# Performance work log

Measured on AMD Instinct MI355X. Metric: run time of the kernel, lower is better.

## Reference

```python
import jax, jax.numpy as jnp
import numpy as np

BATCH, INPUTDIM, OUTDIM, GRIDSIZE = 4096, 256, 256, 64


def setup_inputs() -> dict:
    key = jax.random.key(0)
    k1, k2 = jax.random.split(key)
    x = jax.random.normal(k1, (BATCH, INPUTDIM), dtype=jnp.float32)
    # xavier_uniform over (2, outdim, inputdim, gridsize): fan_in = inputdim*gridsize, fan_out = outdim*gridsize
    fan_in = INPUTDIM * GRIDSIZE
    fan_out = OUTDIM * GRIDSIZE
    limit = float(np.sqrt(6.0 / (fan_in + fan_out)))
    fouriercoeffs = jax.random.uniform(
        k2, (2, OUTDIM, INPUTDIM, GRIDSIZE), dtype=jnp.float32,
        minval=-limit, maxval=limit)
    bias = jnp.zeros((1, OUTDIM), dtype=jnp.float32)
    return {"x": x, "fouriercoeffs": fouriercoeffs, "bias": bias}


def reference(x, fouriercoeffs, bias):
    # x: [B, inputdim]; fouriercoeffs: [2, outdim, inputdim, gridsize]; bias: [1, outdim]
    # gridsize_param is clamp/round'ed to an int in torch -> static = initial_gridsize here.
    G = fouriercoeffs.shape[-1]
    k = jnp.arange(1, G + 1, dtype=x.dtype)        # [G] frequencies 1..G
    xk = x[:, :, None] * k                          # [B, inputdim, G]
    c = jnp.cos(xk)                                 # [B, inputdim, G]
    s = jnp.sin(xk)                                 # [B, inputdim, G]
    # Fused contraction over (inputdim, gridsize) -- avoids the naive
    # [B, outdim, inputdim, gridsize] broadcast tensor of the torch code.
    y = (jnp.einsum('big,oig->bo', c, fouriercoeffs[0])
         + jnp.einsum('big,oig->bo', s, fouriercoeffs[1])
         + bias)                                    # [B, outdim]
    return y
```

## Files before the change

kernel.cpp:

```cpp
#include <hip/hip_runtime.h>
#include <hip/hip_bf16.h>


typedef __attribute__((ext_vector_type(8))) short short8;
typedef __attribute__((ext_vector_type(4))) float f32x4;

#define SPLITK 8
#define ICHUNK (256 / SPLITK)

#define INV2PI 0.15915494309189535f

#if __has_builtin(__builtin_amdgcn_cvt_pk_bf16_f32)
typedef __attribute__((ext_vector_type(2))) __bf16 bf16x2_t;
__device__ __forceinline__ unsigned pkbf16(float a, float b) {
    bf16x2_t v = __builtin_amdgcn_cvt_pk_bf16_f32(a, b);
    return __builtin_bit_cast(unsigned, v);
}
#else
__device__ __forceinline__ unsigned pkbf16(float a, float b) {
    unsigned ua = __builtin_bit_cast(unsigned, a) + 0x8000u;
    unsigned ub = __builtin_bit_cast(unsigned, b) + 0x8000u;
    return __builtin_amdgcn_perm(ub, ua, 0x07060302u);
}
#endif

__device__ __forceinline__ void dbl2(float c, float s, float& co, float& so) {
    float t = c + c;
    co = __builtin_fmaf(t, c, -1.f);
    so = t * s;
}
__device__ __forceinline__ void rot2(float c, float s, float cr, float sr,
                                     float& co, float& so) {
    float t = s * sr;
    co = __builtin_fmaf(c, cr, -t);
    float u = s * cr;
    so = __builtin_fmaf(c, sr, u);
}

__device__ __forceinline__ short8 chain8(float m1, float fm1, float f0) {
    unsigned r[4];
    float vp = fm1, v = f0;
    #pragma unroll
    for (int h = 0; h < 4; ++h) {
        float v1 = __builtin_fmaf(m1, v, -vp);
        r[h] = pkbf16(v, v1);
        float v2 = __builtin_fmaf(m1, v1, -v);
        vp = v1; v = v2;
    }
    uint4 u; u.x = r[0]; u.y = r[1]; u.z = r[2]; u.w = r[3];
    return __builtin_bit_cast(short8, u);
}

__device__ __forceinline__ void async_load16(const void* g, void* l) {
    __builtin_amdgcn_global_load_lds(
        (const __attribute__((address_space(1))) unsigned int*)g,
        (__attribute__((address_space(3))) unsigned int*)l,
        16, 0, 0);
}

__global__ void init_out_kernel(float* __restrict__ out, const float* __restrict__ bias) {
    int tid = blockIdx.x * 256 + threadIdx.x;
    float4 b4 = ((const float4*)bias)[tid & 63];
    ((float4*)out)[tid] = b4;
}

__global__ __launch_bounds__(256) void convert_coeffs3(
    const float* __restrict__ fc, unsigned short* __restrict__ ws2)
{
    unsigned flat = blockIdx.x * 256 + threadIdx.x;
    unsigned bx = flat >> 11, gi = flat & 2047;
    unsigned i = bx >> 1, y = bx & 1;
    unsigned sog = gi >> 6, ll = gi & 63;
    unsigned s = sog >> 3, og = sog & 7;
    unsigned op = og * 16 + (ll & 15);
    unsigned k = s * 32 + ((ll >> 4) * 8);
    unsigned tt = k >> 6, g0 = k & 63;
    const float4* src = (const float4*)(fc +
        ((((size_t)tt * 256 + y * 128 + op) * 256 + i) * 64 + g0));
    float4 a = src[0], b = src[1];
    uint4 v;
    v.x = pkbf16(a.x, a.y); v.y = pkbf16(a.z, a.w);
    v.z = pkbf16(b.x, b.y); v.w = pkbf16(b.z, b.w);
    ((uint4*)ws2)[flat] = v;
}

template <bool USE_WS>
__global__ __launch_bounds__(256, 2) void fkan_gemm(
    const float* __restrict__ x, const float* __restrict__ fc,
    const unsigned short* __restrict__ bws, float* __restrict__ out)
{
    __shared__ uint4 Bimg[2][2048];
    __shared__ float xs[ICHUNK][128];

    const int t  = threadIdx.x;
    const int l  = t & 63;
    const int w  = t >> 6;
    const int wr = w >> 1, wc = w & 1;
    const int q  = l >> 4;
    const int m  = l & 15;
    const int rowBase = blockIdx.x * 128;
    const int by      = blockIdx.y;
    const int colBase = by * 128;
    const int iBase   = blockIdx.z * ICHUNK;

    f32x4 acc[4][4];
    #pragma unroll
    for (int a = 0; a < 4; ++a)
        #pragma unroll
        for (int b = 0; b < 4; ++b) acc[a][b] = (f32x4)0.0f;

    auto stageB = [&](int p, int i) {
        if (USE_WS) {
            const unsigned short* base = bws + ((size_t)(i * 2 + by) * 2048) * 8;
            #pragma unroll
            for (int cc = 0; cc < 8; ++cc) {
                int c = cc * 4 + w;
                async_load16(base + (size_t)(c * 64 + l) * 8, (void*)(&Bimg[p][c * 64]));
            }
        } else {
            #pragma unroll
            for (int gg = 0; gg < 8; ++gg) {
                int gi  = gg * 256 + t;
                int sog = gi >> 6, ll = gi & 63;
                int s = sog >> 3, ogb = sog & 7;
                int o = ogb * 16 + (ll & 15);
                int k = s * 32 + (ll >> 4) * 8;
                int tt = k >> 6, g = k & 63;
                const float4* p4 = (const float4*)(fc +
                    ((((size_t)tt * 256 + colBase + o) * 256 + i) * 64 + g));
                float4 a = p4[0], b = p4[1];
                uint4 v;
                v.x = pkbf16(a.x, a.y); v.y = pkbf16(a.z, a.w);
                v.z = pkbf16(b.x, b.y); v.w = pkbf16(b.z, b.w);
                Bimg[p][gi] = v;
            }
        }
    };

    stageB(0, iBase);
    {
        int r = t >> 1, c0 = (t & 1) * 16;
        const float4* px = (const float4*)(x + (size_t)(rowBase + r) * 256 + iBase + c0);
        float4 v0 = px[0], v1 = px[1], v2 = px[2], v3 = px[3];
        float tmp[16] = { v0.x, v0.y, v0.z, v0.w, v1.x, v1.y, v1.z, v1.w,
                          v2.x, v2.y, v2.z, v2.w, v3.x, v3.y, v3.z, v3.w };
        #pragma unroll
        for (int j = 0; j < 16; ++j) xs[c0 + j][r] = tmp[j];
    }
    __syncthreads();

    #pragma unroll 1
    for (int ii = 0; ii < ICHUNK; ++ii) {
        const int p = ii & 1;

        short8 bF[4][4];
        #pragma unroll
        for (int s = 0; s < 4; ++s)
            #pragma unroll
            for (int cf = 0; cf < 4; ++cf)
                bF[s][cf] = __builtin_bit_cast(short8,
                    Bimg[p][(s * 8 + wc * 4 + cf) * 64 + l]);

        if (ii + 1 < ICHUNK) stageB(p ^ 1, iBase + ii + 1);

        short8 aF[4][4];
        #pragma unroll
        for (int rf = 0; rf < 4; ++rf) {
            float xv = xs[ii][wr * 64 + rf * 16 + m];
            float rev = xv * INV2PI;
            float s1 = __builtin_amdgcn_sinf(rev);
            float c1 = __builtin_amdgcn_cosf(rev);
            const float m1 = c1 + c1;
            float c2, s2, c4, s4, c8, s8, c16, s16, c32, s32;
            dbl2(c1, s1, c2, s2);
            dbl2(c2, s2, c4, s4);
            dbl2(c4, s4, c8, s8);
            dbl2(c8, s8, c16, s16);
            dbl2(c16, s16, c32, s32);
            float c24, s24;
            rot2(c16, s16, c8, s8, c24, s24);
            float cq = (q == 0) ? 1.f : (q == 1) ? c8 : (q == 2) ? c16 : c24;
            float sq = (q == 0) ? 0.f : (q == 1) ? s8 : (q == 2) ? s16 : s24;
            float cq1, sq1, cB, sB, cB1, sB1;
            rot2(cq, sq, c1, s1, cq1, sq1);
            rot2(cq, sq, c32, s32, cB, sB);
            rot2(cB, sB, c1, s1, cB1, sB1);
            aF[rf][0] = chain8(m1, cq, cq1);
            aF[rf][1] = chain8(m1, cB, cB1);
            aF[rf][2] = chain8(m1, sq, sq1);
            aF[rf][3] = chain8(m1, sB, sB1);
        }

        #pragma unroll
        for (int s = 0; s < 4; ++s)
            #pragma unroll
            for (int rf = 0; rf < 4; ++rf)
                #pragma unroll
                for (int cf = 0; cf < 4; ++cf)
                    acc[rf][cf] = __builtin_amdgcn_mfma_f32_16x16x32_bf16(
                        aF[rf][s], bF[s][cf], acc[rf][cf], 0, 0, 0);

        __syncthreads();
    }

    const int lr = (l >> 4) * 4;
    const int r0 = rowBase + wr * 64 + lr;
    const int c0 = colBase + wc * 64 + m;
    #pragma unroll
    for (int rf = 0; rf < 4; ++rf)
        #pragma unroll
        for (int cf = 0; cf < 4; ++cf)
            #pragma unroll
            for (int e = 0; e < 4; ++e)
                atomicAdd(out + (size_t)(r0 + rf * 16 + e) * 256 + (c0 + cf * 16),
                          acc[rf][cf][e]);
}

extern "C" void kernel_launch(void* const* d_in, const int* in_sizes, int n_in,
                              void* d_out, int out_size, void* d_ws, size_t ws_size,
                              hipStream_t stream) {
    const float* x    = (const float*)d_in[0];
    const float* fc   = (const float*)d_in[1];
    const float* bias = (const float*)d_in[2];
    float* out = (float*)d_out;
    unsigned short* bws = (unsigned short*)d_ws;

    hipLaunchKernelGGL(init_out_kernel, dim3(1024), dim3(256), 0, stream, out, bias);

    const size_t wsNeed = (size_t)512 * 2048 * 16;
    if (ws_size >= wsNeed) {
        hipLaunchKernelGGL(convert_coeffs3, dim3(4096), dim3(256), 0, stream, fc, bws);
        hipLaunchKernelGGL((fkan_gemm<true>), dim3(32, 2, SPLITK), dim3(256), 0, stream,
                           x, fc, bws, out);
    } else {
        hipLaunchKernelGGL((fkan_gemm<false>), dim3(32, 2, SPLITK), dim3(256), 0, stream,
                           x, fc, bws, out);
    }
}
```

Measured before the change: 181.5 us.

## Widen GEMM tile to all 256 outputs and fuse prep kernels

```diff
diff --git a/kernel.cpp b/kernel.cpp
--- a/kernel.cpp
+++ b/kernel.cpp
@@ -58,38 +58,42 @@
         16, 0, 0);
 }
 
-__global__ void init_out_kernel(float* __restrict__ out, const float* __restrict__ bias) {
-    int tid = blockIdx.x * 256 + threadIdx.x;
-    float4 b4 = ((const float4*)bias)[tid & 63];
-    ((float4*)out)[tid] = b4;
-}
-
-__global__ __launch_bounds__(256) void convert_coeffs3(
-    const float* __restrict__ fc, unsigned short* __restrict__ ws2)
+__global__ __launch_bounds__(256) void prep_kernel(
+    const float* __restrict__ fc, const float* __restrict__ bias,
+    unsigned short* __restrict__ ws2, float* __restrict__ out)
 {
-    unsigned flat = blockIdx.x * 256 + threadIdx.x;
-    unsigned bx = flat >> 11, gi = flat & 2047;
-    unsigned i = bx >> 1, y = bx & 1;
-    unsigned sog = gi >> 6, ll = gi & 63;
-    unsigned s = sog >> 3, og = sog & 7;
-    unsigned op = og * 16 + (ll & 15);
-    unsigned k = s * 32 + ((ll >> 4) * 8);
-    unsigned tt = k >> 6, g0 = k & 63;
-    const float4* src = (const float4*)(fc +
-        ((((size_t)tt * 256 + y * 128 + op) * 256 + i) * 64 + g0));
-    float4 a = src[0], b = src[1];
-    uint4 v;
-    v.x = pkbf16(a.x, a.y); v.y = pkbf16(a.z, a.w);
-    v.z = pkbf16(b.x, b.y); v.w = pkbf16(b.z, b.w);
-    ((uint4*)ws2)[flat] = v;
+    const int bid = blockIdx.x;
+    const int t = threadIdx.x;
+    if (bid < 2048) {
+        const int i = bid >> 3, s = (bid >> 1) & 3, h = bid & 1;
+        const int o = t;
+        const int ka = s * 32 + h * 16;
+        const int tt = ka >> 6, g0 = ka & 63;
+        const float4* src = (const float4*)(fc +
+            ((((size_t)tt * 256 + o) * 256 + i) * 64 + g0));
+        float4 a = src[0], b = src[1], c = src[2], d = src[3];
+        uint4 vA, vB;
+        vA.x = pkbf16(a.x, a.y); vA.y = pkbf16(a.z, a.w);
+        vA.z = pkbf16(b.x, b.y); vA.w = pkbf16(b.z, b.w);
+        vB.x = pkbf16(c.x, c.y); vB.y = pkbf16(c.z, c.w);
+        vB.z = pkbf16(d.x, d.y); vB.w = pkbf16(d.z, d.w);
+        uint4* dst = (uint4*)ws2 + ((size_t)i * 4096 +
+                     (size_t)(s * 16 + (o >> 4)) * 64 + h * 32 + (o & 15));
+        dst[0]  = vA;
+        dst[16] = vB;
+    } else {
+        int tid = (bid - 2048) * 256 + t;
+        float4 b4 = ((const float4*)bias)[tid & 63];
+        ((float4*)out)[tid] = b4;
+    }
 }
 
 template <bool USE_WS>
-__global__ __launch_bounds__(256, 2) void fkan_gemm(
+__global__ __launch_bounds__(256, 1) void fkan_gemm(
     const float* __restrict__ x, const float* __restrict__ fc,
     const unsigned short* __restrict__ bws, float* __restrict__ out)
 {
-    __shared__ uint4 Bimg[2][2048];
+    __shared__ uint4 Bimg[2][4096];
     __shared__ float xs[ICHUNK][128];
 
     const int t  = threadIdx.x;
@@ -99,35 +103,33 @@
     const int q  = l >> 4;
     const int m  = l & 15;
     const int rowBase = blockIdx.x * 128;
-    const int by      = blockIdx.y;
-    const int colBase = by * 128;
     const int iBase   = blockIdx.z * ICHUNK;
 
-    f32x4 acc[4][4];
+    f32x4 acc[4][8];
     #pragma unroll
     for (int a = 0; a < 4; ++a)
         #pragma unroll
-        for (int b = 0; b < 4; ++b) acc[a][b] = (f32x4)0.0f;
+        for (int b = 0; b < 8; ++b) acc[a][b] = (f32x4)0.0f;
 
     auto stageB = [&](int p, int i) {
         if (USE_WS) {
-            const unsigned short* base = bws + ((size_t)(i * 2 + by) * 2048) * 8;
-            #pragma unroll
-            for (int cc = 0; cc < 8; ++cc) {
+            const uint4* base = (const uint4*)bws + (size_t)i * 4096;
+            #pragma unroll
+            for (int cc = 0; cc < 16; ++cc) {
                 int c = cc * 4 + w;
-                async_load16(base + (size_t)(c * 64 + l) * 8, (void*)(&Bimg[p][c * 64]));
+                async_load16(base + (size_t)c * 64 + l, (void*)(&Bimg[p][c * 64]));
             }
         } else {
             #pragma unroll
-            for (int gg = 0; gg < 8; ++gg) {
+            for (int gg = 0; gg < 16; ++gg) {
                 int gi  = gg * 256 + t;
                 int sog = gi >> 6, ll = gi & 63;
-                int s = sog >> 3, ogb = sog & 7;
-                int o = ogb * 16 + (ll & 15);
+                int s = sog >> 4, og = sog & 15;
+                int o = og * 16 + (ll & 15);
                 int k = s * 32 + (ll >> 4) * 8;
                 int tt = k >> 6, g = k & 63;
                 const float4* p4 = (const float4*)(fc +
-                    ((((size_t)tt * 256 + colBase + o) * 256 + i) * 64 + g));
+                    ((((size_t)tt * 256 + o) * 256 + i) * 64 + g));
                 float4 a = p4[0], b = p4[1];
                 uint4 v;
                 v.x = pkbf16(a.x, a.y); v.y = pkbf16(a.z, a.w);
@@ -152,14 +154,6 @@
     #pragma unroll 1
     for (int ii = 0; ii < ICHUNK; ++ii) {
         const int p = ii & 1;
-
-        short8 bF[4][4];
-        #pragma unroll
-        for (int s = 0; s < 4; ++s)
-            #pragma unroll
-            for (int cf = 0; cf < 4; ++cf)
-                bF[s][cf] = __builtin_bit_cast(short8,
-                    Bimg[p][(s * 8 + wc * 4 + cf) * 64 + l]);
 
         if (ii + 1 < ICHUNK) stageB(p ^ 1, iBase + ii + 1);
 
@@ -191,25 +185,37 @@
             aF[rf][3] = chain8(m1, sB, sB1);
         }
 
-        #pragma unroll
-        for (int s = 0; s < 4; ++s)
+        short8 bFc[8], bFn[8];
+        #pragma unroll
+        for (int cf = 0; cf < 8; ++cf)
+            bFc[cf] = __builtin_bit_cast(short8, Bimg[p][(wc * 8 + cf) * 64 + l]);
+        #pragma unroll
+        for (int s = 0; s < 4; ++s) {
+            if (s < 3) {
+                #pragma unroll
+                for (int cf = 0; cf < 8; ++cf)
+                    bFn[cf] = __builtin_bit_cast(short8,
+                        Bimg[p][((s + 1) * 16 + wc * 8 + cf) * 64 + l]);
+            }
             #pragma unroll
             for (int rf = 0; rf < 4; ++rf)
                 #pragma unroll
-                for (int cf = 0; cf < 4; ++cf)
+                for (int cf = 0; cf < 8; ++cf)
                     acc[rf][cf] = __builtin_amdgcn_mfma_f32_16x16x32_bf16(
-                        aF[rf][s], bF[s][cf], acc[rf][cf], 0, 0, 0);
+                        aF[rf][s], bFc[cf], acc[rf][cf], 0, 0, 0);
+            #pragma unroll
+            for (int cf = 0; cf < 8; ++cf) bFc[cf] = bFn[cf];
+        }
 
         __syncthreads();
     }
 
-    const int lr = (l >> 4) * 4;
-    const int r0 = rowBase + wr * 64 + lr;
-    const int c0 = colBase + wc * 64 + m;
+    const int r0 = rowBase + wr * 64 + (l >> 4) * 4;
+    const int c0 = wc * 128 + m;
     #pragma unroll
     for (int rf = 0; rf < 4; ++rf)
         #pragma unroll
-        for (int cf = 0; cf < 4; ++cf)
+        for (int cf = 0; cf < 8; ++cf)
             #pragma unroll
             for (int e = 0; e < 4; ++e)
                 atomicAdd(out + (size_t)(r0 + rf * 16 + e) * 256 + (c0 + cf * 16),
@@ -225,15 +231,16 @@
     float* out = (float*)d_out;
     unsigned short* bws = (unsigned short*)d_ws;
 
-    hipLaunchKernelGGL(init_out_kernel, dim3(1024), dim3(256), 0, stream, out, bias);
-
-    const size_t wsNeed = (size_t)512 * 2048 * 16;
+    const size_t wsNeed = (size_t)256 * 4096 * 16;
     if (ws_size >= wsNeed) {
-        hipLaunchKernelGGL(convert_coeffs3, dim3(4096), dim3(256), 0, stream, fc, bws);
-        hipLaunchKernelGGL((fkan_gemm<true>), dim3(32, 2, SPLITK), dim3(256), 0, stream,
+        hipLaunchKernelGGL(prep_kernel, dim3(3072), dim3(256), 0, stream,
+                           fc, bias, bws, out);
+        hipLaunchKernelGGL((fkan_gemm<true>), dim3(32, 1, SPLITK), dim3(256), 0, stream,
                            x, fc, bws, out);
     } else {
-        hipLaunchKernelGGL((fkan_gemm<false>), dim3(32, 2, SPLITK), dim3(256), 0, stream,
+        hipLaunchKernelGGL(prep_kernel, dim3(3072), dim3(256), 0, stream,
+                           fc, bias, bws, out);
+        hipLaunchKernelGGL((fkan_gemm<false>), dim3(32, 1, SPLITK), dim3(256), 0, stream,
                            x, fc, bws, out);
     }
 }
```

Result: slower. 185.5 us (+2.2%).
